# Kernel tuning notes

Hardware: AMD Instinct MI355X
Metric: run time of the kernel (lower is better)

Reference implementation:

```python
import jax, jax.numpy as jnp
import numpy as np

# Model dims (from init_kwargs + mamba_ssm defaults)
D_MODEL = 1024
N_LAYER = 2
D_STATE = 16
D_CONV = 4
D_INNER = 2 * D_MODEL          # expand=2
DT_RANK = D_MODEL // 16        # 64
VOCAB = 32000
BATCH, SEQLEN = 2, 1024


def setup_inputs() -> dict:
    key = jax.random.key(0)
    ks = jax.random.split(key, 10)
    s = 0.02
    x = jax.random.randint(ks[0], (BATCH, SEQLEN), 0, VOCAB)
    embedding = jax.random.normal(ks[1], (VOCAB, D_MODEL), dtype=jnp.float32) * s
    norm_w = jnp.ones((N_LAYER, D_MODEL), dtype=jnp.float32)
    in_proj_w = jax.random.normal(ks[2], (N_LAYER, 2 * D_INNER, D_MODEL), dtype=jnp.float32) * s
    conv_w = jax.random.normal(ks[3], (N_LAYER, D_INNER, D_CONV), dtype=jnp.float32) * (1.0 / np.sqrt(D_CONV))
    conv_b = jnp.zeros((N_LAYER, D_INNER), dtype=jnp.float32)
    x_proj_w = jax.random.normal(ks[4], (N_LAYER, DT_RANK + 2 * D_STATE, D_INNER), dtype=jnp.float32) * s
    dt_proj_w = jax.random.normal(ks[5], (N_LAYER, D_INNER, DT_RANK), dtype=jnp.float32) * (DT_RANK ** -0.5)
    # inverse-softplus of dt_init ~ 0.01 (mamba default dt range)
    dt_bias = jnp.full((N_LAYER, D_INNER), float(np.log(np.expm1(0.01))), dtype=jnp.float32)
    A_log = jnp.log(jnp.broadcast_to(jnp.arange(1, D_STATE + 1, dtype=jnp.float32), (N_LAYER, D_INNER, D_STATE)))
    D = jnp.ones((N_LAYER, D_INNER), dtype=jnp.float32)
    out_proj_w = jax.random.normal(ks[6], (N_LAYER, D_MODEL, D_INNER), dtype=jnp.float32) * s
    final_norm_w = jnp.ones((D_MODEL,), dtype=jnp.float32)
    return {"x": x, "embedding": embedding, "norm_w": norm_w, "in_proj_w": in_proj_w,
            "conv_w": conv_w, "conv_b": conv_b, "x_proj_w": x_proj_w, "dt_proj_w": dt_proj_w,
            "dt_bias": dt_bias, "A_log": A_log, "D": D, "out_proj_w": out_proj_w,
            "final_norm_w": final_norm_w}


def _rmsnorm(h, w, eps=1e-5):
    return h * jax.lax.rsqrt(jnp.mean(h * h, axis=-1, keepdims=True) + eps) * w


def _scan_combine(c1, c2):
    a1, b1 = c1
    a2, b2 = c2
    return a2 * a1, a2 * b1 + b2


def _mamba_block(h, norm_w, in_proj_w, conv_w, conv_b, x_proj_w, dt_proj_w, dt_bias, A_log, D, out_proj_w):
    u = _rmsnorm(h, norm_w)
    xz = jnp.einsum('bld,ed->ble', u, in_proj_w)           # [B,L,2*D_INNER]
    xi, z = jnp.split(xz, 2, axis=-1)
    # depthwise causal conv1d, kernel D_CONV
    k = conv_w.T[:, None, :]                               # [D_CONV, 1, D_INNER]
    xc = jax.lax.conv_general_dilated(xi, k, (1,), [(D_CONV - 1, 0)],
                                      dimension_numbers=('NLC', 'LIO', 'NLC'),
                                      feature_group_count=D_INNER) + conv_b
    xc = jax.nn.silu(xc)
    dbl = jnp.einsum('bld,ed->ble', xc, x_proj_w)          # [B,L,DT_RANK+2*D_STATE]
    dt_low = dbl[..., :DT_RANK]
    Bm = dbl[..., DT_RANK:DT_RANK + D_STATE]
    Cm = dbl[..., DT_RANK + D_STATE:]
    dt = jax.nn.softplus(jnp.einsum('blr,dr->bld', dt_low, dt_proj_w) + dt_bias)
    A = -jnp.exp(A_log)                                    # [D_INNER, D_STATE]
    a = jnp.exp(dt[..., None] * A)                         # [B,L,D_INNER,D_STATE]
    b = dt[..., None] * Bm[:, :, None, :] * xc[..., None]  # [B,L,D_INNER,D_STATE]
    hs = jax.lax.associative_scan(_scan_combine, (a, b), axis=1)[1]
    y = jnp.einsum('bldn,bln->bld', hs, Cm) + xc * D
    y = y * jax.nn.silu(z)
    return h + jnp.einsum('bld,md->blm', y, out_proj_w)


def reference(x, embedding, norm_w, in_proj_w, conv_w, conv_b, x_proj_w, dt_proj_w,
              dt_bias, A_log, D, out_proj_w, final_norm_w):
    h = embedding[x]                                       # [B,L,D_MODEL]
    for i in range(N_LAYER):
        h = _mamba_block(h, norm_w[i], in_proj_w[i], conv_w[i], conv_b[i], x_proj_w[i],
                         dt_proj_w[i], dt_bias[i], A_log[i], D[i], out_proj_w[i])
    h = _rmsnorm(h, final_norm_w)
    logits = jnp.einsum('bld,vd->blv', h, embedding)       # tied lm head
    return logits
```

## Files before the change

kernel.cpp:

```cpp
#include <hip/hip_runtime.h>
#include <hip/hip_bf16.h>
#include <math.h>

#define D_MODEL 1024
#define N_LAYER 2
#define D_STATE 16
#define D_CONV  4
#define D_INNER 2048
#define DT_RANK 64
#define VOCAB   32000
#define BATCH   2
#define SEQLEN  1024
#define TOKENS  (BATCH*SEQLEN)
#define NC      64
#define CL      16
#define XPZ     16

typedef __hip_bfloat16 bf16;
typedef __bf16 bf16x8 __attribute__((ext_vector_type(8)));
typedef float f32x4 __attribute__((ext_vector_type(4)));

__device__ inline void gld_lds16(const bf16* g, bf16* l) {
    __builtin_amdgcn_global_load_lds(
        (const __attribute__((address_space(1))) void*)g,
        (__attribute__((address_space(3))) void*)l, 16, 0, 0);
}

__device__ inline float softplus_fast(float v) {
    return (v > 20.f) ? v : __logf(1.f + __expf(v));
}
__device__ inline float silu_fast(float v) {
    return v / (1.f + __expf(-v));
}
__device__ inline float bfu(unsigned short s) {
    unsigned u = ((unsigned)s) << 16;
    float f;
    __builtin_memcpy(&f, &u, 4);
    return f;
}
__device__ inline unsigned short bfb(float v) {
    bf16 b = __float2bfloat16(v);
    unsigned short s;
    __builtin_memcpy(&s, &b, 2);
    return s;
}

__global__ __launch_bounds__(256) void embed_rms(const int* __restrict__ x,
                                                 const float* __restrict__ emb,
                                                 const float* __restrict__ w,
                                                 float* __restrict__ h,
                                                 bf16* __restrict__ u) {
    int t = blockIdx.x;
    int tok = x[t];
    float4 v = ((const float4*)(emb + (size_t)tok * D_MODEL))[threadIdx.x];
    ((float4*)(h + (size_t)t * D_MODEL))[threadIdx.x] = v;
    float ss = v.x*v.x + v.y*v.y + v.z*v.z + v.w*v.w;
    #pragma unroll
    for (int off = 32; off > 0; off >>= 1) ss += __shfl_down(ss, off);
    __shared__ float red[4];
    int lane = threadIdx.x & 63, wid = threadIdx.x >> 6;
    if (lane == 0) red[wid] = ss;
    __syncthreads();
    float tot = red[0] + red[1] + red[2] + red[3];
    float scale = rsqrtf(tot * (1.0f / (float)D_MODEL) + 1e-5f);
    float4 wq = ((const float4*)w)[threadIdx.x];
    size_t o = (size_t)t * D_MODEL + threadIdx.x * 4;
    u[o+0] = __float2bfloat16(v.x * scale * wq.x);
    u[o+1] = __float2bfloat16(v.y * scale * wq.y);
    u[o+2] = __float2bfloat16(v.z * scale * wq.z);
    u[o+3] = __float2bfloat16(v.w * scale * wq.w);
}

__global__ __launch_bounds__(256) void f32_to_bf16(const float* __restrict__ s,
                                                   bf16* __restrict__ d, int n) {
    int i = (blockIdx.x * 256 + threadIdx.x) * 4;
    if (i < n) {
        float4 v = *(const float4*)(s + i);
        d[i+0] = __float2bfloat16(v.x);
        d[i+1] = __float2bfloat16(v.y);
        d[i+2] = __float2bfloat16(v.z);
        d[i+3] = __float2bfloat16(v.w);
    }
}

__global__ __launch_bounds__(256) void conv_xproj_pad(const float* __restrict__ s,
                                                      bf16* __restrict__ d) {
    int col = blockIdx.x * 256 + threadIdx.x;
    int row = blockIdx.y;
    int layer = blockIdx.z;
    float v = (row < 96) ? s[((size_t)layer * 96 + row) * D_INNER + col] : 0.f;
    d[((size_t)layer * 128 + row) * D_INNER + col] = __float2bfloat16(v);
}

__global__ __launch_bounds__(256) void gemm_bf16(
    const bf16* __restrict__ A, int lda,
    const bf16* __restrict__ W, int ldw,
    float* __restrict__ C, int ldc,
    int N, int K, int acc, int swz, int M, int bfout)
{
    __shared__ bf16 lds[2][2][128 * 64];
    int bx = blockIdx.x, by = blockIdx.y;
    if (swz) {
        int bid = by * gridDim.x + bx;
        int q = (gridDim.x * gridDim.y) >> 3;
        int n = (bid & 7) * q + (bid >> 3);
        by = n % gridDim.y;
        bx = n / gridDim.y;
    }
    const int z = blockIdx.z;
    A += (size_t)z * K;
    W += (size_t)z * K;
    float* Cf = C + (size_t)z * M * (size_t)ldc;
    bf16*  Cb = (bf16*)C + (size_t)z * M * (size_t)ldc;

    const int tid  = threadIdx.x;
    const int wave = tid >> 6;
    const int lane = tid & 63;
    const int wr = wave >> 1, wc = wave & 1;
    const size_t rowBase = (size_t)by * 128;
    const size_t colBase = (size_t)bx * 128;

    const int srow = 8 * wave + (lane >> 3);
    const int scol = ((lane & 7) ^ (lane >> 3)) << 3;
    const bf16* aGs = A + (rowBase + srow) * (size_t)lda + scol;
    const bf16* bGs = W + (colBase + srow) * (size_t)ldw + scol;

#define STAGE(tt, bb) do {                                                      \
        const size_t kofs_ = (size_t)(tt) * 64;                                 \
        _Pragma("unroll")                                                       \
        for (int i_ = 0; i_ < 4; ++i_) {                                        \
            gld_lds16(aGs + kofs_ + (size_t)(32 * i_) * lda,                    \
                      &lds[bb][0][(32 * i_ + 8 * wave) * 64]);                  \
            gld_lds16(bGs + kofs_ + (size_t)(32 * i_) * ldw,                    \
                      &lds[bb][1][(32 * i_ + 8 * wave) * 64]);                  \
        }                                                                       \
    } while (0)

    f32x4 accv[4][4];
    #pragma unroll
    for (int i = 0; i < 4; ++i)
        #pragma unroll
        for (int j = 0; j < 4; ++j)
            accv[i][j] = f32x4{0.f, 0.f, 0.f, 0.f};

    const int arow0 = wr * 64 + (lane & 15);
    const int brow0 = wc * 64 + (lane & 15);
    const int h8  = (lane >> 4) << 3;
    const int sw8 = (lane & 7) << 3;

    const int NT = K >> 6;
    STAGE(0, 0);
    for (int t = 0; t < NT; ++t) {
        const int cur = t & 1;
        if (t + 1 < NT) {
            STAGE(t + 1, cur ^ 1);
            asm volatile("s_waitcnt vmcnt(8)" ::: "memory");
        } else {
            asm volatile("s_waitcnt vmcnt(0)" ::: "memory");
        }
        __builtin_amdgcn_s_barrier();

        const bf16* Ab = &lds[cur][0][0];
        const bf16* Bb = &lds[cur][1][0];
        #pragma unroll
        for (int kk = 0; kk < 2; ++kk) {
            const int cs = ((kk << 5) + h8) ^ sw8;
            bf16x8 af[4], bv[4];
            #pragma unroll
            for (int i = 0; i < 4; ++i)
                af[i] = *(const bf16x8*)(Ab + (arow0 + 16 * i) * 64 + cs);
            #pragma unroll
            for (int j = 0; j < 4; ++j)
                bv[j] = *(const bf16x8*)(Bb + (brow0 + 16 * j) * 64 + cs);
            #pragma unroll
            for (int i = 0; i < 4; ++i)
                #pragma unroll
                for (int j = 0; j < 4; ++j)
                    accv[i][j] = __builtin_amdgcn_mfma_f32_16x16x32_bf16(
                        af[i], bv[j], accv[i][j], 0, 0, 0);
        }
        asm volatile("s_waitcnt lgkmcnt(0)" ::: "memory");
        __builtin_amdgcn_s_barrier();
    }
#undef STAGE

    const int cl = lane & 15;
    const int rg = (lane >> 4) * 4;
    #pragma unroll
    for (int i = 0; i < 4; ++i) {
        #pragma unroll
        for (int j = 0; j < 4; ++j) {
            int col = (int)colBase + wc * 64 + j * 16 + cl;
            if (col < N) {
                size_t base = (rowBase + wr * 64 + i * 16 + rg) * (size_t)ldc + col;
                if (bfout) {
                    #pragma unroll
                    for (int r = 0; r < 4; ++r)
                        Cb[base + (size_t)r * ldc] = __float2bfloat16(accv[i][j][r]);
                } else {
                    #pragma unroll
                    for (int r = 0; r < 4; ++r) {
                        size_t idx = base + (size_t)r * ldc;
                        Cf[idx] = acc ? Cf[idx] + accv[i][j][r] : accv[i][j][r];
                    }
                }
            }
        }
    }
}

__global__ __launch_bounds__(512) void gemm_wide3(
    const bf16* __restrict__ A,
    const bf16* __restrict__ W,
    float* __restrict__ C, int ldc, int bfout)
{
    __shared__ bf16 ldsA[3][256 * 32];
    __shared__ bf16 ldsB[3][128 * 32];
    int bx = blockIdx.x, by = blockIdx.y;
    {
        int bid = by * gridDim.x + bx;
        int n = (bid & 7) * ((gridDim.x * gridDim.y) >> 3) + (bid >> 3);
        by = n & 7;
        bx = n >> 3;
    }
    const int tid  = threadIdx.x;
    const int wave = tid >> 6;
    const int lane = tid & 63;
    const int wr = wave >> 1;
    const int wc = wave & 1;
    const size_t rowBase = (size_t)by * 256;
    const size_t colBase = (size_t)bx * 128;

    const int srow   = lane >> 2;
    const int schunk = ((lane & 3) ^ ((lane >> 3) & 3)) << 3;
    const bf16* aG0 = A + (rowBase + 16 * wave       + srow) * (size_t)D_MODEL + schunk;
    const bf16* aG1 = A + (rowBase + 128 + 16 * wave + srow) * (size_t)D_MODEL + schunk;
    const bf16* bG  = W + (colBase + 16 * wave       + srow) * (size_t)D_MODEL + schunk;

#define STAGEW(tt, sAp, sBp) do {                                               \
        const size_t ko_ = (size_t)(tt) * 32;                                   \
        gld_lds16(aG0 + ko_, (sAp) + 512 * wave);                               \
        gld_lds16(aG1 + ko_, (sAp) + 512 * (8 + wave));                         \
        gld_lds16(bG  + ko_, (sBp) + 512 * wave);                               \
    } while (0)

    f32x4 accv[4][4];
    #pragma unroll
    for (int i = 0; i < 4; ++i)
        #pragma unroll
        for (int j = 0; j < 4; ++j)
            accv[i][j] = f32x4{0.f, 0.f, 0.f, 0.f};

    const int l15 = lane & 15;
    const int cs = (((lane >> 4) ^ ((l15 >> 1) & 3)) << 3);
    const int arow0 = wr * 64 + l15;
    const int brow0 = wc * 64 + l15;

    STAGEW(0, &ldsA[0][0], &ldsB[0][0]);
    STAGEW(1, &ldsA[1][0], &ldsB[1][0]);

    int rs = 0, ps = 2;
    #pragma unroll 1
    for (int t = 0; t < 32; ++t) {
        if (t < 31) { asm volatile("s_waitcnt vmcnt(3)" ::: "memory"); }
        else        { asm volatile("s_waitcnt vmcnt(0)" ::: "memory"); }
        __builtin_amdgcn_s_barrier();
        __builtin_amdgcn_sched_barrier(0);

        if (t + 2 < 32) STAGEW(t + 2, &ldsA[ps][0], &ldsB[ps][0]);

        const bf16* Ab = &ldsA[rs][0];
        const bf16* Bb = &ldsB[rs][0];
        bf16x8 af[4], bv[4];
        #pragma unroll
        for (int i = 0; i < 4; ++i)
            af[i] = *(const bf16x8*)(Ab + (arow0 + 16 * i) * 32 + cs);
        #pragma unroll
        for (int j = 0; j < 4; ++j)
            bv[j] = *(const bf16x8*)(Bb + (brow0 + 16 * j) * 32 + cs);
        #pragma unroll
        for (int i = 0; i < 4; ++i)
            #pragma unroll
            for (int j = 0; j < 4; ++j)
                accv[i][j] = __builtin_amdgcn_mfma_f32_16x16x32_bf16(
                    af[i], bv[j], accv[i][j], 0, 0, 0);

        rs = (rs == 2) ? 0 : rs + 1;
        ps = (ps == 2) ? 0 : ps + 1;
    }
#undef STAGEW

    const int cl = l15;
    const int rg = (lane >> 4) * 4;
    #pragma unroll
    for (int i = 0; i < 4; ++i) {
        #pragma unroll
        for (int j = 0; j < 4; ++j) {
            int col = (int)colBase + wc * 64 + j * 16 + cl;
            size_t base = (rowBase + wr * 64 + i * 16 + rg) * (size_t)ldc + col;
            if (bfout) {
                bf16* Cb = (bf16*)C;
                #pragma unroll
                for (int r = 0; r < 4; ++r)
                    Cb[base + (size_t)r * ldc] = __float2bfloat16(accv[i][j][r]);
            } else {
                #pragma unroll
                for (int r = 0; r < 4; ++r)
                    C[base + (size_t)r * ldc] = accv[i][j][r];
            }
        }
    }
}

__global__ __launch_bounds__(256) void conv_silu_kernel(const bf16* __restrict__ xz,
                                                        const float* __restrict__ cw,
                                                        const float* __restrict__ cb,
                                                        bf16* __restrict__ xcb) {
    int d  = (blockIdx.x * 256 + threadIdx.x) * 2;
    int l0 = blockIdx.y * 8;
    int b  = blockIdx.z;
    float4 wa = *(const float4*)(cw + d * 4);
    float4 wb = *(const float4*)(cw + d * 4 + 4);
    float2 bias = *(const float2*)(cb + d);
    const bf16* base = xz + (size_t)b * SEQLEN * (2 * D_INNER) + d;

    float a0 = 0.f, a1 = 0.f, a2 = 0.f;
    float b0 = 0.f, b1 = 0.f, b2 = 0.f;
    #pragma unroll
    for (int j = 0; j < 3; ++j) {
        int l = l0 - 3 + j;
        float va = 0.f, vb = 0.f;
        if (l >= 0) {
            unsigned v;
            __builtin_memcpy(&v, base + (size_t)l * (2 * D_INNER), 4);
            va = bfu((unsigned short)v);
            vb = bfu((unsigned short)(v >> 16));
        }
        if (j == 0) { a0 = va; b0 = vb; }
        else if (j == 1) { a1 = va; b1 = vb; }
        else { a2 = va; b2 = vb; }
    }
    #pragma unroll
    for (int i = 0; i < 8; ++i) {
        unsigned v;
        __builtin_memcpy(&v, base + (size_t)(l0 + i) * (2 * D_INNER), 4);
        float ca = bfu((unsigned short)v);
        float cbv = bfu((unsigned short)(v >> 16));
        float sa = silu_fast(bias.x + wa.x * a0 + wa.y * a1 + wa.z * a2 + wa.w * ca);
        float sb = silu_fast(bias.y + wb.x * b0 + wb.y * b1 + wb.z * b2 + wb.w * cbv);
        unsigned o = (unsigned)bfb(sa) | ((unsigned)bfb(sb) << 16);
        unsigned* dst = (unsigned*)(xcb + ((size_t)b * SEQLEN + l0 + i) * D_INNER + d);
        *dst = o;
        a0 = a1; a1 = a2; a2 = ca;
        b0 = b1; b1 = b2; b2 = cbv;
    }
}

__global__ __launch_bounds__(256) void reduce_xproj(const bf16* __restrict__ px,
                                                    bf16* __restrict__ dbl_b) {
    int i = blockIdx.x * 256 + threadIdx.x;
    float s = 0.f;
    #pragma unroll
    for (int z = 0; z < XPZ; ++z) {
        unsigned short v;
        __builtin_memcpy(&v, px + (size_t)z * (TOKENS * 96) + i, 2);
        s += bfu(v);
    }
    dbl_b[i] = __float2bfloat16(s);
}

__global__ __launch_bounds__(256) void reduce_oproj_rms(const bf16* __restrict__ po,
                                                        float* __restrict__ h,
                                                        const float* __restrict__ w,
                                                        bf16* __restrict__ u) {
    int t = blockIdx.x;
    size_t base = (size_t)t * D_MODEL + threadIdx.x * 4;
    ushort4 ua = *(const ushort4*)(po + base);
    ushort4 ub = *(const ushort4*)(po + (size_t)TOKENS * D_MODEL + base);
    float4 hv = *(const float4*)(h + base);
    hv.x += bfu(ua.x) + bfu(ub.x);
    hv.y += bfu(ua.y) + bfu(ub.y);
    hv.z += bfu(ua.z) + bfu(ub.z);
    hv.w += bfu(ua.w) + bfu(ub.w);
    *(float4*)(h + base) = hv;
    float ss = hv.x*hv.x + hv.y*hv.y + hv.z*hv.z + hv.w*hv.w;
    #pragma unroll
    for (int off = 32; off > 0; off >>= 1) ss += __shfl_down(ss, off);
    __shared__ float red[4];
    int lane = threadIdx.x & 63, wid = threadIdx.x >> 6;
    if (lane == 0) red[wid] = ss;
    __syncthreads();
    float tot = red[0] + red[1] + red[2] + red[3];
    float scale = rsqrtf(tot * (1.0f / (float)D_MODEL) + 1e-5f);
    float4 wq = ((const float4*)w)[threadIdx.x];
    u[base+0] = __float2bfloat16(hv.x * scale * wq.x);
    u[base+1] = __float2bfloat16(hv.y * scale * wq.y);
    u[base+2] = __float2bfloat16(hv.z * scale * wq.z);
    u[base+3] = __float2bfloat16(hv.w * scale * wq.w);
}

__global__ __launch_bounds__(256) void scan_chunk(const bf16* __restrict__ dtp,
                                                  const float* __restrict__ dt_bias,
                                                  const bf16* __restrict__ dbl,
                                                  const bf16* __restrict__ xc,
                                                  const float* __restrict__ A_log,
                                                  float* __restrict__ dts_out,
                                                  bf16* __restrict__ sfin) {
    int d = blockIdx.x * 256 + threadIdx.x;
    int c = blockIdx.y;
    int b = blockIdx.z;
    __shared__ float Bs[CL][D_STATE];
    {
        int i = threadIdx.x;
        int l = i >> 4, n = i & 15;
        Bs[l][n] = __bfloat162float(dbl[((size_t)b * SEQLEN + c * CL + l) * 96 + DT_RANK + n]);
    }
    __syncthreads();
    float A[D_STATE];
    #pragma unroll
    for (int n = 0; n < D_STATE; ++n) A[n] = -__expf(A_log[d * D_STATE + n]);
    float bias = dt_bias[d];
    float st[D_STATE];
    #pragma unroll
    for (int n = 0; n < D_STATE; ++n) st[n] = 0.f;
    float dts = 0.f;
    for (int l = 0; l < CL; ++l) {
        size_t t = (size_t)b * SEQLEN + c * CL + l;
        float dtv = softplus_fast(__bfloat162float(dtp[t * D_INNER + d]) + bias);
        dts += dtv;
        float dx = dtv * __bfloat162float(xc[t * D_INNER + d]);
        #pragma unroll
        for (int n = 0; n < D_STATE; ++n) {
            float a = __expf(dtv * A[n]);
            st[n] = a * st[n] + dx * Bs[l][n];
        }
    }
    dts_out[((size_t)b * NC + c) * D_INNER + d] = dts;
    #pragma unroll
    for (int n = 0; n < D_STATE; ++n) {
        size_t o = (((size_t)b * NC + c) * D_STATE + n) * D_INNER + d;
        sfin[o] = __float2bfloat16(st[n]);
    }
}

__global__ __launch_bounds__(256) void scan_carry(const float* __restrict__ dts,
                                                  const bf16* __restrict__ sfin,
                                                  const float* __restrict__ A_log,
                                                  bf16* __restrict__ initS) {
    int idx = blockIdx.x * 256 + threadIdx.x;
    int d = idx & (D_INNER - 1);
    int n = (idx >> 11) & (D_STATE - 1);
    int b = idx >> 15;
    float A = -__expf(A_log[d * D_STATE + n]);
    float st = 0.f;
    for (int c = 0; c < NC; ++c) {
        size_t o = (((size_t)b * NC + c) * D_STATE + n) * D_INNER + d;
        initS[o] = __float2bfloat16(st);
        float ap = __expf(dts[((size_t)b * NC + c) * D_INNER + d] * A);
        st = ap * st + __bfloat162float(sfin[o]);
    }
}

__global__ __launch_bounds__(256) void scan_emit(const bf16* __restrict__ dtp,
                                                 const float* __restrict__ dt_bias,
                                                 const bf16* __restrict__ dbl,
                                                 const bf16* __restrict__ xc,
                                                 const bf16* __restrict__ xz,
                                                 const float* __restrict__ A_log,
                                                 const float* __restrict__ Dp,
                                                 const bf16* __restrict__ initS,
                                                 bf16* __restrict__ y) {
    int d = blockIdx.x * 256 + threadIdx.x;
    int c = blockIdx.y;
    int b = blockIdx.z;
    __shared__ float BCs[CL][2 * D_STATE];
    for (int i = threadIdx.x; i < CL * 2 * D_STATE; i += 256) {
        int l = i >> 5, n = i & 31;
        BCs[l][n] = __bfloat162float(dbl[((size_t)b * SEQLEN + c * CL + l) * 96 + DT_RANK + n]);
    }
    __syncthreads();
    float A[D_STATE];
    #pragma unroll
    for (int n = 0; n < D_STATE; ++n) A[n] = -__expf(A_log[d * D_STATE + n]);
    float bias = dt_bias[d];
    float Dv = Dp[d];
    float st[D_STATE];
    #pragma unroll
    for (int n = 0; n < D_STATE; ++n)
        st[n] = __bfloat162float(initS[(((size_t)b * NC + c) * D_STATE + n) * D_INNER + d]);
    for (int l = 0; l < CL; ++l) {
        size_t t = (size_t)b * SEQLEN + c * CL + l;
        float dtv = softplus_fast(__bfloat162float(dtp[t * D_INNER + d]) + bias);
        float xcv = __bfloat162float(xc[t * D_INNER + d]);
        float dx = dtv * xcv;
        float acc = 0.f;
        #pragma unroll
        for (int n = 0; n < D_STATE; ++n) {
            float a = __expf(dtv * A[n]);
            st[n] = a * st[n] + dx * BCs[l][n];
            acc += st[n] * BCs[l][D_STATE + n];
        }
        acc += xcv * Dv;
        float zv = __bfloat162float(xz[t * (2 * D_INNER) + D_INNER + d]);
        y[t * D_INNER + d] = __float2bfloat16(acc * silu_fast(zv));
    }
}

extern "C" void kernel_launch(void* const* d_in, const int* in_sizes, int n_in,
                              void* d_out, int out_size, void* d_ws, size_t ws_size,
                              hipStream_t stream) {
    const int*   x          = (const int*)  d_in[0];
    const float* emb        = (const float*)d_in[1];
    const float* norm_w     = (const float*)d_in[2];
    const float* in_proj_w  = (const float*)d_in[3];
    const float* conv_w     = (const float*)d_in[4];
    const float* conv_b     = (const float*)d_in[5];
    const float* x_proj_w   = (const float*)d_in[6];
    const float* dt_proj_w  = (const float*)d_in[7];
    const float* dt_bias    = (const float*)d_in[8];
    const float* A_log      = (const float*)d_in[9];
    const float* Dp         = (const float*)d_in[10];
    const float* out_proj_w = (const float*)d_in[11];
    const float* fnorm_w    = (const float*)d_in[12];
    float* out = (float*)d_out;
    float* ws  = (float*)d_ws;

    bf16*  embf   = (bf16*)ws;
    bf16*  u_b    = (bf16*)(ws + 16384000);
    bf16*  xz_b   = (bf16*)(ws + 17432576);
    bf16*  dtp_b  = (bf16*)(ws + 25821184);
    bf16*  xc_b   = (bf16*)(ws + 30015488);
    float* h      = ws + 36306944;
    bf16*  dbl_b  = (bf16*)(ws + 38600704);
    bf16*  y_b    = (bf16*)(ws + 38699008);
    bf16*  inpj_b = (bf16*)(ws + 40796160);
    bf16*  xpj_b  = (bf16*)(ws + 44990464);
    bf16*  dtpj_b = (bf16*)(ws + 45252608);
    bf16*  otpj_b = (bf16*)(ws + 45383680);
    float* dts    = ws + 47480832;
    bf16*  sfin   = (bf16*)(ws + 49577984);
    bf16*  initS  = (bf16*)(ws + 51675136);
    bf16*  px_b   = (bf16*)(ws + 53772288);
    bf16*  po_b   = (bf16*)(ws + 56918016);

    f32_to_bf16<<<(VOCAB*D_MODEL/4 + 255)/256, 256, 0, stream>>>(emb, embf, VOCAB*D_MODEL);
    f32_to_bf16<<<(2*2*D_INNER*D_MODEL/4 + 255)/256, 256, 0, stream>>>(in_proj_w,  inpj_b, 2*2*D_INNER*D_MODEL);
    conv_xproj_pad<<<dim3(D_INNER/256, 128, N_LAYER), 256, 0, stream>>>(x_proj_w, xpj_b);
    f32_to_bf16<<<(2*D_INNER*DT_RANK/4 + 255)/256, 256, 0, stream>>>(dt_proj_w,  dtpj_b, 2*D_INNER*DT_RANK);
    f32_to_bf16<<<(2*D_MODEL*D_INNER/4 + 255)/256, 256, 0, stream>>>(out_proj_w, otpj_b, 2*D_MODEL*D_INNER);

    embed_rms<<<TOKENS, 256, 0, stream>>>(x, emb, norm_w, h, u_b);

    for (int layer = 0; layer < N_LAYER; ++layer) {
        gemm_wide3<<<dim3(4096/128, TOKENS/256), 512, 0, stream>>>(
            u_b, inpj_b + (size_t)layer * 2 * D_INNER * D_MODEL,
            (float*)xz_b, 2 * D_INNER, 1);
        conv_silu_kernel<<<dim3(D_INNER/512, SEQLEN/8, BATCH), 256, 0, stream>>>(
            xz_b, conv_w + (size_t)layer * D_INNER * D_CONV, conv_b + layer * D_INNER,
            xc_b);
        gemm_bf16<<<dim3(1, TOKENS/128, XPZ), 256, 0, stream>>>(
            xc_b, D_INNER, xpj_b + (size_t)layer * 128 * D_INNER, D_INNER,
            (float*)px_b, 96, 96, 128, 0, 0, TOKENS, 1);
        reduce_xproj<<<(TOKENS*96)/256, 256, 0, stream>>>(px_b, dbl_b);
        gemm_bf16<<<dim3(D_INNER/128, TOKENS/128), 256, 0, stream>>>(
            dbl_b, 96, dtpj_b + (size_t)layer * D_INNER * DT_RANK, DT_RANK,
            (float*)dtp_b, D_INNER, D_INNER, DT_RANK, 0, 1, TOKENS, 1);
        scan_chunk<<<dim3(D_INNER/256, NC, BATCH), 256, 0, stream>>>(
            dtp_b, dt_bias + layer * D_INNER, dbl_b, xc_b,
            A_log + (size_t)layer * D_INNER * D_STATE, dts, sfin);
        scan_carry<<<(BATCH*D_STATE*D_INNER)/256, 256, 0, stream>>>(
            dts, sfin, A_log + (size_t)layer * D_INNER * D_STATE, initS);
        scan_emit<<<dim3(D_INNER/256, NC, BATCH), 256, 0, stream>>>(
            dtp_b, dt_bias + layer * D_INNER, dbl_b, xc_b, xz_b,
            A_log + (size_t)layer * D_INNER * D_STATE, Dp + layer * D_INNER,
            initS, y_b);
        gemm_bf16<<<dim3(D_MODEL/128, TOKENS/128, 2), 256, 0, stream>>>(
            y_b, D_INNER, otpj_b + (size_t)layer * D_MODEL * D_INNER, D_INNER,
            (float*)po_b, D_MODEL, D_MODEL, 1024, 0, 1, TOKENS, 1);
        reduce_oproj_rms<<<TOKENS, 256, 0, stream>>>(
            po_b, h, (layer + 1 < N_LAYER) ? (norm_w + (layer + 1) * D_MODEL) : fnorm_w,
            u_b);
    }

    gemm_wide3<<<dim3(VOCAB/128, TOKENS/256), 512, 0, stream>>>(u_b, embf, out, VOCAB, 0);
}
```

Measured before the change: 506.9 us.

## Fuse chunked selective scan into one kernel with in-block LDS prefix scan

```diff
diff --git a/kernel.cpp b/kernel.cpp
--- a/kernel.cpp
+++ b/kernel.cpp
@@ -399,110 +399,97 @@
     u[base+3] = __float2bfloat16(hv.w * scale * wq.w);
 }
 
-__global__ __launch_bounds__(256) void scan_chunk(const bf16* __restrict__ dtp,
+__global__ __launch_bounds__(256) void scan_fused(const bf16* __restrict__ dtp,
                                                   const float* __restrict__ dt_bias,
                                                   const bf16* __restrict__ dbl,
                                                   const bf16* __restrict__ xc,
+                                                  const bf16* __restrict__ xz,
                                                   const float* __restrict__ A_log,
-                                                  float* __restrict__ dts_out,
-                                                  bf16* __restrict__ sfin) {
-    int d = blockIdx.x * 256 + threadIdx.x;
-    int c = blockIdx.y;
-    int b = blockIdx.z;
-    __shared__ float Bs[CL][D_STATE];
-    {
-        int i = threadIdx.x;
-        int l = i >> 4, n = i & 15;
-        Bs[l][n] = __bfloat162float(dbl[((size_t)b * SEQLEN + c * CL + l) * 96 + DT_RANK + n]);
-    }
-    __syncthreads();
+                                                  const float* __restrict__ Dp,
+                                                  bf16* __restrict__ y) {
+    const int d_sub = threadIdx.x >> 6;
+    const int c     = threadIdx.x & 63;
+    const int d     = blockIdx.x * 4 + d_sub;
+    const int b     = blockIdx.y;
+
     float A[D_STATE];
     #pragma unroll
     for (int n = 0; n < D_STATE; ++n) A[n] = -__expf(A_log[d * D_STATE + n]);
-    float bias = dt_bias[d];
+    const float bias = dt_bias[d];
+
+    const size_t t0 = (size_t)b * SEQLEN + c * CL;
+    const bf16* drow = dbl + t0 * 96 + DT_RANK;
+
     float st[D_STATE];
     #pragma unroll
     for (int n = 0; n < D_STATE; ++n) st[n] = 0.f;
     float dts = 0.f;
     for (int l = 0; l < CL; ++l) {
-        size_t t = (size_t)b * SEQLEN + c * CL + l;
-        float dtv = softplus_fast(__bfloat162float(dtp[t * D_INNER + d]) + bias);
+        float dtv = softplus_fast(__bfloat162float(dtp[(t0 + l) * D_INNER + d]) + bias);
         dts += dtv;
-        float dx = dtv * __bfloat162float(xc[t * D_INNER + d]);
+        float dx = dtv * __bfloat162float(xc[(t0 + l) * D_INNER + d]);
+        bf16x8 B0 = *(const bf16x8*)(drow + l * 96);
+        bf16x8 B1 = *(const bf16x8*)(drow + l * 96 + 8);
         #pragma unroll
         for (int n = 0; n < D_STATE; ++n) {
             float a = __expf(dtv * A[n]);
-            st[n] = a * st[n] + dx * Bs[l][n];
-        }
-    }
-    dts_out[((size_t)b * NC + c) * D_INNER + d] = dts;
-    #pragma unroll
-    for (int n = 0; n < D_STATE; ++n) {
-        size_t o = (((size_t)b * NC + c) * D_STATE + n) * D_INNER + d;
-        sfin[o] = __float2bfloat16(st[n]);
-    }
-}
-
-__global__ __launch_bounds__(256) void scan_carry(const float* __restrict__ dts,
-                                                  const bf16* __restrict__ sfin,
-                                                  const float* __restrict__ A_log,
-                                                  bf16* __restrict__ initS) {
-    int idx = blockIdx.x * 256 + threadIdx.x;
-    int d = idx & (D_INNER - 1);
-    int n = (idx >> 11) & (D_STATE - 1);
-    int b = idx >> 15;
-    float A = -__expf(A_log[d * D_STATE + n]);
-    float st = 0.f;
-    for (int c = 0; c < NC; ++c) {
-        size_t o = (((size_t)b * NC + c) * D_STATE + n) * D_INNER + d;
-        initS[o] = __float2bfloat16(st);
-        float ap = __expf(dts[((size_t)b * NC + c) * D_INNER + d] * A);
-        st = ap * st + __bfloat162float(sfin[o]);
-    }
-}
-
-__global__ __launch_bounds__(256) void scan_emit(const bf16* __restrict__ dtp,
-                                                 const float* __restrict__ dt_bias,
-                                                 const bf16* __restrict__ dbl,
-                                                 const bf16* __restrict__ xc,
-                                                 const bf16* __restrict__ xz,
-                                                 const float* __restrict__ A_log,
-                                                 const float* __restrict__ Dp,
-                                                 const bf16* __restrict__ initS,
-                                                 bf16* __restrict__ y) {
-    int d = blockIdx.x * 256 + threadIdx.x;
-    int c = blockIdx.y;
-    int b = blockIdx.z;
-    __shared__ float BCs[CL][2 * D_STATE];
-    for (int i = threadIdx.x; i < CL * 2 * D_STATE; i += 256) {
-        int l = i >> 5, n = i & 31;
-        BCs[l][n] = __bfloat162float(dbl[((size_t)b * SEQLEN + c * CL + l) * 96 + DT_RANK + n]);
-    }
+            float Bv = (n < 8) ? (float)B0[n] : (float)B1[n - 8];
+            st[n] = a * st[n] + dx * Bv;
+        }
+    }
+    float ap[D_STATE];
+    #pragma unroll
+    for (int n = 0; n < D_STATE; ++n) ap[n] = __expf(dts * A[n]);
+
+    __shared__ float sA_[4][64][D_STATE];
+    __shared__ float sS_[4][64][D_STATE];
+    #pragma unroll 1
+    for (int off = 1; off < 64; off <<= 1) {
+        #pragma unroll
+        for (int n = 0; n < D_STATE; ++n) {
+            sA_[d_sub][c][n] = ap[n];
+            sS_[d_sub][c][n] = st[n];
+        }
+        __syncthreads();
+        if (c >= off) {
+            #pragma unroll
+            for (int n = 0; n < D_STATE; ++n) {
+                float pa = sA_[d_sub][c - off][n];
+                float ps = sS_[d_sub][c - off][n];
+                st[n] = ap[n] * ps + st[n];
+                ap[n] = ap[n] * pa;
+            }
+        }
+        __syncthreads();
+    }
+    #pragma unroll
+    for (int n = 0; n < D_STATE; ++n) sS_[d_sub][c][n] = st[n];
     __syncthreads();
-    float A[D_STATE];
-    #pragma unroll
-    for (int n = 0; n < D_STATE; ++n) A[n] = -__expf(A_log[d * D_STATE + n]);
-    float bias = dt_bias[d];
-    float Dv = Dp[d];
-    float st[D_STATE];
     #pragma unroll
     for (int n = 0; n < D_STATE; ++n)
-        st[n] = __bfloat162float(initS[(((size_t)b * NC + c) * D_STATE + n) * D_INNER + d]);
+        st[n] = (c == 0) ? 0.f : sS_[d_sub][c - 1][n];
+
+    const float Dv = Dp[d];
     for (int l = 0; l < CL; ++l) {
-        size_t t = (size_t)b * SEQLEN + c * CL + l;
-        float dtv = softplus_fast(__bfloat162float(dtp[t * D_INNER + d]) + bias);
-        float xcv = __bfloat162float(xc[t * D_INNER + d]);
+        float dtv = softplus_fast(__bfloat162float(dtp[(t0 + l) * D_INNER + d]) + bias);
+        float xcv = __bfloat162float(xc[(t0 + l) * D_INNER + d]);
         float dx = dtv * xcv;
+        bf16x8 B0 = *(const bf16x8*)(drow + l * 96);
+        bf16x8 B1 = *(const bf16x8*)(drow + l * 96 + 8);
+        bf16x8 C0 = *(const bf16x8*)(drow + l * 96 + 16);
+        bf16x8 C1 = *(const bf16x8*)(drow + l * 96 + 24);
         float acc = 0.f;
         #pragma unroll
         for (int n = 0; n < D_STATE; ++n) {
             float a = __expf(dtv * A[n]);
-            st[n] = a * st[n] + dx * BCs[l][n];
-            acc += st[n] * BCs[l][D_STATE + n];
+            float Bv = (n < 8) ? (float)B0[n] : (float)B1[n - 8];
+            float Cv = (n < 8) ? (float)C0[n] : (float)C1[n - 8];
+            st[n] = a * st[n] + dx * Bv;
+            acc += st[n] * Cv;
         }
         acc += xcv * Dv;
-        float zv = __bfloat162float(xz[t * (2 * D_INNER) + D_INNER + d]);
-        y[t * D_INNER + d] = __float2bfloat16(acc * silu_fast(zv));
+        float zv = __bfloat162float(xz[(t0 + l) * (2 * D_INNER) + D_INNER + d]);
+        y[(t0 + l) * D_INNER + d] = __float2bfloat16(acc * silu_fast(zv));
     }
 }
 
@@ -537,9 +524,6 @@
     bf16*  xpj_b  = (bf16*)(ws + 44990464);
     bf16*  dtpj_b = (bf16*)(ws + 45252608);
     bf16*  otpj_b = (bf16*)(ws + 45383680);
-    float* dts    = ws + 47480832;
-    bf16*  sfin   = (bf16*)(ws + 49577984);
-    bf16*  initS  = (bf16*)(ws + 51675136);
     bf16*  px_b   = (bf16*)(ws + 53772288);
     bf16*  po_b   = (bf16*)(ws + 56918016);
 
@@ -565,15 +549,9 @@
         gemm_bf16<<<dim3(D_INNER/128, TOKENS/128), 256, 0, stream>>>(
             dbl_b, 96, dtpj_b + (size_t)layer * D_INNER * DT_RANK, DT_RANK,
             (float*)dtp_b, D_INNER, D_INNER, DT_RANK, 0, 1, TOKENS, 1);
-        scan_chunk<<<dim3(D_INNER/256, NC, BATCH), 256, 0, stream>>>(
-            dtp_b, dt_bias + layer * D_INNER, dbl_b, xc_b,
-            A_log + (size_t)layer * D_INNER * D_STATE, dts, sfin);
-        scan_carry<<<(BATCH*D_STATE*D_INNER)/256, 256, 0, stream>>>(
-            dts, sfin, A_log + (size_t)layer * D_INNER * D_STATE, initS);
-        scan_emit<<<dim3(D_INNER/256, NC, BATCH), 256, 0, stream>>>(
+        scan_fused<<<dim3(D_INNER/4, BATCH), 256, 0, stream>>>(
             dtp_b, dt_bias + layer * D_INNER, dbl_b, xc_b, xz_b,
-            A_log + (size_t)layer * D_INNER * D_STATE, Dp + layer * D_INNER,
-            initS, y_b);
+            A_log + (size_t)layer * D_INNER * D_STATE, Dp + layer * D_INNER, y_b);
         gemm_bf16<<<dim3(D_MODEL/128, TOKENS/128, 2), 256, 0, stream>>>(
             y_b, D_INNER, otpj_b + (size_t)layer * D_MODEL * D_INNER, D_INNER,
             (float*)po_b, D_MODEL, D_MODEL, 1024, 0, 1, TOKENS, 1);
```

After: 701.0 us. +38.3%, slower.
